# Kernel optimization log

Measured on AMD Instinct MI355X. Metric: run time of the kernel, lower is better.

The kernel has to match this reference:

```python
import jax, jax.numpy as jnp
import numpy as np

TOKENS = 8192
IN_FEATURES = 4096
OUT_FEATURES = 4096
ALPHA = 2e-05
BETA = 8.0


def setup_inputs() -> dict:
    key = jax.random.key(0)
    kx, kw = jax.random.split(key)
    # int8 activations and weights, values in [-127, 127]
    x = jax.random.randint(kx, (TOKENS, IN_FEATURES), -127, 128, dtype=jnp.int32).astype(jnp.int8)
    weight = jax.random.randint(kw, (OUT_FEATURES, IN_FEATURES), -127, 128, dtype=jnp.int32).astype(jnp.int8)
    bias = jnp.zeros((OUT_FEATURES,), dtype=jnp.float32)
    a = jnp.float32(ALPHA)  # dequant scale: input_scale * weight_scale
    b = jnp.float32(BETA)   # requant scale: 1 / out_scale
    return {"x": x, "weight": weight, "bias": bias, "a": a, "b": b}


def reference(x, weight, bias, a, b):
    acc = jnp.matmul(x.astype(jnp.int32), weight.T.astype(jnp.int32))
    # fp32 epilogue: dequant scale + bias, exact GeLU, requant by beta
    y = a * acc.astype(jnp.float32) + bias[None, :]
    y = jax.nn.gelu(y, approximate=False)
    # quantize output to int8 (round to nearest even, saturate)
    q = jnp.clip(jnp.rint(y * b), -128.0, 127.0).astype(jnp.int8)
    return q
```

## Files before the change

kernel.cpp:

```cpp
#include <hip/hip_runtime.h>
#include <cstdint>
#include <cstddef>

#define TOKENS 8192
#define INF    4096
#define OUTF   4096

typedef int v4i __attribute__((ext_vector_type(4)));

__global__ __launch_bounds__(256) void pack_i8_kernel(
    const int* __restrict__ xi, const int* __restrict__ wi,
    uint8_t* __restrict__ x8, uint8_t* __restrict__ w8) {
  const int NXT = (TOKENS * INF) / 16;
  const int NT  = 2048 * 256;
  int tid = blockIdx.x * 256 + threadIdx.x;
#pragma unroll 1
  for (int g = 0; g < 6; ++g) {
    int t = g * NT + tid;
    const int4* s;
    int4* d;
    if (t < NXT) {
      s = (const int4*)xi + 4 * (size_t)t;
      d = (int4*)x8 + t;
    } else {
      int t2 = t - NXT;
      s = (const int4*)wi + 4 * (size_t)t2;
      d = (int4*)w8 + t2;
    }
    int4 v0 = s[0], v1 = s[1], v2 = s[2], v3 = s[3];
    int4 p;
    p.x = (v0.x & 255) | ((v0.y & 255) << 8) | ((v0.z & 255) << 16) | (v0.w << 24);
    p.y = (v1.x & 255) | ((v1.y & 255) << 8) | ((v1.z & 255) << 16) | (v1.w << 24);
    p.z = (v2.x & 255) | ((v2.y & 255) << 8) | ((v2.z & 255) << 16) | (v2.w << 24);
    p.w = (v3.x & 255) | ((v3.y & 255) << 8) | ((v3.z & 255) << 16) | (v3.w << 24);
    *d = p;
  }
}

__device__ __forceinline__ float gelu_exact(float y) {
  float x = y * 0.70710678118654752f;
  float s = fabsf(x);
  float t = __builtin_amdgcn_rcpf(fmaf(s, 0.3275911f, 1.0f));
  float p = t * fmaf(t, fmaf(t, fmaf(t, fmaf(t, 1.061405429f, -1.453152027f),
                                     1.421413741f), -0.284496736f),
                     0.254829592f);
  float e = __expf(-s * s);
  float er = fmaf(-p, e, 1.0f);
  er = copysignf(er, x);
  return 0.5f * y * (1.0f + er);
}

__device__ __forceinline__ void barrier_fenced() {
  asm volatile("" ::: "memory");
  __builtin_amdgcn_s_barrier();
  asm volatile("" ::: "memory");
}

__global__ __launch_bounds__(512, 2) void gemm_i8_gelu_q_kernel(
    const uint8_t* __restrict__ x8, const uint8_t* __restrict__ w8,
    const float* __restrict__ bias, const float* __restrict__ pa,
    const float* __restrict__ pb, int* __restrict__ out) {
  __shared__ char sm[131072];

  const int tid = threadIdx.x;
  const int l   = tid & 63;
  const int wv  = tid >> 6;
  const int wr  = wv >> 2;
  const int wc  = wv & 3;
  const int lr  = l & 15;
  const int lg  = l >> 4;

  int id = blockIdx.x;
  int wg = (id & 7) * 64 + (id >> 3);
  const int m0 = (wg >> 4) * 256;
  const int n0 = (wg & 15) * 256;

  const float av = pa[0];
  const float bv = pb[0];

  const int grow = (wv << 5) + (l >> 3);
  const int gch  = ((l & 7) ^ ((l >> 3) & 7)) << 4;
  const uint8_t* gA = x8 + (size_t)(m0 + grow) * INF + gch;
  const uint8_t* gB = w8 + (size_t)(n0 + grow) * INF + gch;
  const int dwv = wv * 4096;

  int aoff[8], boff[4], sb0, sb1;
#pragma unroll
  for (int m = 0; m < 8; ++m) aoff[m] = (wr * 128 + m * 16 + lr) * 128;
#pragma unroll
  for (int n = 0; n < 4; ++n) boff[n] = 32768 + (wc * 64 + n * 16 + lr) * 128;
  sb0 = ((0 + lg) ^ (l & 7)) << 4;
  sb1 = ((4 + lg) ^ (l & 7)) << 4;

  v4i acc[8][4];
#pragma unroll
  for (int m = 0; m < 8; ++m)
#pragma unroll
    for (int n = 0; n < 4; ++n) acc[m][n] = (v4i){0, 0, 0, 0};

#define GLL(gsrc, ldst)                                                       \
  __builtin_amdgcn_global_load_lds(                                           \
      (const __attribute__((address_space(1))) unsigned*)(gsrc),              \
      (__attribute__((address_space(3))) unsigned*)(ldst), 16, 0, 0);

#define GLA(T, J) GLL(gA + (size_t)(J) * 8 * INF + (size_t)(T) * 128,         \
                      sm + (((T) & 1) << 16) + dwv + (J) * 1024)
#define GLB(T, J) GLL(gB + (size_t)(J) * 8 * INF + (size_t)(T) * 128,         \
                      sm + (((T) & 1) << 16) + 32768 + dwv + (J) * 1024)

#define LD(off) (*(const v4i*)(sbr + (off)))
#define MM(ACC, AF, BF)                                                       \
  ACC = __builtin_amdgcn_mfma_i32_16x16x64_i8(AF, BF, ACC, 0, 0, 0)

#define KSTEP                                                                 \
  __builtin_amdgcn_s_setprio(1);                                              \
  MM(acc[0][0], A0[0], B0[0]); MM(acc[0][1], A0[0], B0[1]);                   \
  MM(acc[1][0], A0[1], B0[0]); MM(acc[1][1], A0[1], B0[1]);                   \
  MM(acc[2][0], A0[2], B0[0]); MM(acc[2][1], A0[2], B0[1]);                   \
  MM(acc[3][0], A0[3], B0[0]); MM(acc[3][1], A0[3], B0[1]);                   \
  __builtin_amdgcn_s_setprio(0);                                              \
  __builtin_amdgcn_s_setprio(1);                                              \
  MM(acc[4][0], A4[0], B0[0]); MM(acc[4][1], A4[0], B0[1]);                   \
  MM(acc[5][0], A4[1], B0[0]); MM(acc[5][1], A4[1], B0[1]);                   \
  MM(acc[6][0], A4[2], B0[0]); MM(acc[6][1], A4[2], B0[1]);                   \
  MM(acc[7][0], A4[3], B0[0]); MM(acc[7][1], A4[3], B0[1]);                   \
  __builtin_amdgcn_s_setprio(0);                                              \
  __builtin_amdgcn_s_setprio(1);                                              \
  MM(acc[0][2], A0[0], B2[0]); MM(acc[0][3], A0[0], B2[1]);                   \
  MM(acc[1][2], A0[1], B2[0]); MM(acc[1][3], A0[1], B2[1]);                   \
  MM(acc[2][2], A0[2], B2[0]); MM(acc[2][3], A0[2], B2[1]);                   \
  MM(acc[3][2], A0[3], B2[0]); MM(acc[3][3], A0[3], B2[1]);                   \
  __builtin_amdgcn_s_setprio(0);                                              \
  __builtin_amdgcn_s_setprio(1);                                              \
  MM(acc[4][2], A4[0], B2[0]); MM(acc[4][3], A4[0], B2[1]);                   \
  MM(acc[5][2], A4[1], B2[0]); MM(acc[5][3], A4[1], B2[1]);                   \
  MM(acc[6][2], A4[2], B2[0]); MM(acc[6][3], A4[2], B2[1]);                   \
  MM(acc[7][2], A4[3], B2[0]); MM(acc[7][3], A4[3], B2[1]);                   \
  __builtin_amdgcn_s_setprio(0);

#define ITER(DS)                                                              \
  {                                                                           \
    const char* sbr = sm + ((kt & 1) << 16);                                  \
    const int T = kt + 1;                                                     \
    v4i A0[4], A4[4], B0[2], B2[2];                                           \
        \
    A0[0] = LD(aoff[0] + sb0); A0[1] = LD(aoff[1] + sb0);                     \
    A0[2] = LD(aoff[2] + sb0); A0[3] = LD(aoff[3] + sb0);                     \
    B0[0] = LD(boff[0] + sb0); B0[1] = LD(boff[1] + sb0);                     \
    if (DS) {                                                                 \
      GLA(T, 0); GLA(T, 1); GLA(T, 2); GLA(T, 3);                             \
      GLB(T, 0); GLB(T, 1); GLB(T, 2); GLB(T, 3);                             \
    }                                                                         \
    A4[0] = LD(aoff[4] + sb0); A4[1] = LD(aoff[5] + sb0);                     \
    A4[2] = LD(aoff[6] + sb0); A4[3] = LD(aoff[7] + sb0);                     \
    B2[0] = LD(boff[2] + sb0); B2[1] = LD(boff[3] + sb0);                     \
    KSTEP                                                                     \
    A0[0] = LD(aoff[0] + sb1); A0[1] = LD(aoff[1] + sb1);                     \
    A0[2] = LD(aoff[2] + sb1); A0[3] = LD(aoff[3] + sb1);                     \
    B0[0] = LD(boff[0] + sb1); B0[1] = LD(boff[1] + sb1);                     \
    A4[0] = LD(aoff[4] + sb1); A4[1] = LD(aoff[5] + sb1);                     \
    A4[2] = LD(aoff[6] + sb1); A4[3] = LD(aoff[7] + sb1);                     \
    B2[0] = LD(boff[2] + sb1); B2[1] = LD(boff[3] + sb1);                     \
    KSTEP                                                                     \
          \
    if (DS) { asm volatile("s_waitcnt vmcnt(0)" ::: "memory"); }              \
    barrier_fenced();                                                         \
  }

  GLA(0, 0); GLA(0, 1); GLA(0, 2); GLA(0, 3);
  GLB(0, 0); GLB(0, 1); GLB(0, 2); GLB(0, 3);
  asm volatile("s_waitcnt vmcnt(0)" ::: "memory");
  barrier_fenced();

#pragma unroll 1
  for (int kt = 0; kt < 31; ++kt) ITER(1)
  {
    const int kt = 31;
    ITER(0)
  }

  float bvals[4];
#pragma unroll
  for (int n = 0; n < 4; ++n) bvals[n] = bias[n0 + wc * 64 + n * 16 + lr];

#pragma unroll
  for (int m = 0; m < 8; ++m) {
    int rowb = m0 + wr * 128 + m * 16 + lg * 4;
#pragma unroll
    for (int q = 0; q < 4; ++q) {
      size_t rb = (size_t)(rowb + q) * OUTF;
#pragma unroll
      for (int n = 0; n < 4; ++n) {
        float f = fmaf(av, (float)acc[m][n][q], bvals[n]);
        float g = gelu_exact(f);
        float r = __builtin_rintf(g * bv);
        r = fminf(fmaxf(r, -128.0f), 127.0f);
        out[rb + (size_t)(n0 + wc * 64 + n * 16 + lr)] = (int)r;
      }
    }
  }
#undef GLL
#undef GLA
#undef GLB
#undef LD
#undef MM
#undef KSTEP
#undef ITER
}

extern "C" void kernel_launch(void* const* d_in, const int* in_sizes, int n_in,
                              void* d_out, int out_size, void* d_ws,
                              size_t ws_size, hipStream_t stream) {
  const int*   xi   = (const int*)d_in[0];
  const int*   wi   = (const int*)d_in[1];
  const float* bias = (const float*)d_in[2];
  const float* pa   = (const float*)d_in[3];
  const float* pb   = (const float*)d_in[4];
  int*         out  = (int*)d_out;

  uint8_t* x8 = (uint8_t*)d_ws;
  uint8_t* w8 = x8 + (size_t)TOKENS * INF;

  pack_i8_kernel<<<2048, 256, 0, stream>>>(xi, wi, x8, w8);

  dim3 grid((TOKENS / 256) * (OUTF / 256));
  gemm_i8_gelu_q_kernel<<<grid, 512, 0, stream>>>(x8, w8, bias, pa, pb, out);
}
```

Measured before the change: 388.0 us.

## Interleave LDS fragment loads with MFMA clusters and pin schedule with group barriers

Moves the wait-and-barrier to the start of each k-tile iteration, so the global-to-LDS prefetch for the next tile is issued right after the barrier. The second half-step's A/B fragment loads are split and interleaved between MFMA clusters using separate register sets. sched_group_barrier directives pin the order of global loads, LDS reads and MFMAs. The aim is to hide LDS read latency behind matrix work, at the cost of more live vector registers, which could reduce occupancy or cause spills.

```diff
diff --git a/kernel.cpp b/kernel.cpp
--- a/kernel.cpp
+++ b/kernel.cpp
@@ -112,65 +112,58 @@
 #define MM(ACC, AF, BF)                                                       \
   ACC = __builtin_amdgcn_mfma_i32_16x16x64_i8(AF, BF, ACC, 0, 0, 0)
 
-#define KSTEP                                                                 \
+#define CL(AF, BF, MB, NB)                                                    \
   __builtin_amdgcn_s_setprio(1);                                              \
-  MM(acc[0][0], A0[0], B0[0]); MM(acc[0][1], A0[0], B0[1]);                   \
-  MM(acc[1][0], A0[1], B0[0]); MM(acc[1][1], A0[1], B0[1]);                   \
-  MM(acc[2][0], A0[2], B0[0]); MM(acc[2][1], A0[2], B0[1]);                   \
-  MM(acc[3][0], A0[3], B0[0]); MM(acc[3][1], A0[3], B0[1]);                   \
-  __builtin_amdgcn_s_setprio(0);                                              \
-  __builtin_amdgcn_s_setprio(1);                                              \
-  MM(acc[4][0], A4[0], B0[0]); MM(acc[4][1], A4[0], B0[1]);                   \
-  MM(acc[5][0], A4[1], B0[0]); MM(acc[5][1], A4[1], B0[1]);                   \
-  MM(acc[6][0], A4[2], B0[0]); MM(acc[6][1], A4[2], B0[1]);                   \
-  MM(acc[7][0], A4[3], B0[0]); MM(acc[7][1], A4[3], B0[1]);                   \
-  __builtin_amdgcn_s_setprio(0);                                              \
-  __builtin_amdgcn_s_setprio(1);                                              \
-  MM(acc[0][2], A0[0], B2[0]); MM(acc[0][3], A0[0], B2[1]);                   \
-  MM(acc[1][2], A0[1], B2[0]); MM(acc[1][3], A0[1], B2[1]);                   \
-  MM(acc[2][2], A0[2], B2[0]); MM(acc[2][3], A0[2], B2[1]);                   \
-  MM(acc[3][2], A0[3], B2[0]); MM(acc[3][3], A0[3], B2[1]);                   \
-  __builtin_amdgcn_s_setprio(0);                                              \
-  __builtin_amdgcn_s_setprio(1);                                              \
-  MM(acc[4][2], A4[0], B2[0]); MM(acc[4][3], A4[0], B2[1]);                   \
-  MM(acc[5][2], A4[1], B2[0]); MM(acc[5][3], A4[1], B2[1]);                   \
-  MM(acc[6][2], A4[2], B2[0]); MM(acc[6][3], A4[2], B2[1]);                   \
-  MM(acc[7][2], A4[3], B2[0]); MM(acc[7][3], A4[3], B2[1]);                   \
+  MM(acc[(MB)+0][(NB)+0], AF[0], BF[0]); MM(acc[(MB)+0][(NB)+1], AF[0], BF[1]);\
+  MM(acc[(MB)+1][(NB)+0], AF[1], BF[0]); MM(acc[(MB)+1][(NB)+1], AF[1], BF[1]);\
+  MM(acc[(MB)+2][(NB)+0], AF[2], BF[0]); MM(acc[(MB)+2][(NB)+1], AF[2], BF[1]);\
+  MM(acc[(MB)+3][(NB)+0], AF[3], BF[0]); MM(acc[(MB)+3][(NB)+1], AF[3], BF[1]);\
   __builtin_amdgcn_s_setprio(0);
 
 #define ITER(DS)                                                              \
   {                                                                           \
     const char* sbr = sm + ((kt & 1) << 16);                                  \
     const int T = kt + 1;                                                     \
-    v4i A0[4], A4[4], B0[2], B2[2];                                           \
-        \
-    A0[0] = LD(aoff[0] + sb0); A0[1] = LD(aoff[1] + sb0);                     \
-    A0[2] = LD(aoff[2] + sb0); A0[3] = LD(aoff[3] + sb0);                     \
-    B0[0] = LD(boff[0] + sb0); B0[1] = LD(boff[1] + sb0);                     \
+    asm volatile("s_waitcnt vmcnt(0)" ::: "memory");      \
+    barrier_fenced();           \
     if (DS) {                                                                 \
       GLA(T, 0); GLA(T, 1); GLA(T, 2); GLA(T, 3);                             \
       GLB(T, 0); GLB(T, 1); GLB(T, 2); GLB(T, 3);                             \
     }                                                                         \
-    A4[0] = LD(aoff[4] + sb0); A4[1] = LD(aoff[5] + sb0);                     \
-    A4[2] = LD(aoff[6] + sb0); A4[3] = LD(aoff[7] + sb0);                     \
-    B2[0] = LD(boff[2] + sb0); B2[1] = LD(boff[3] + sb0);                     \
-    KSTEP                                                                     \
-    A0[0] = LD(aoff[0] + sb1); A0[1] = LD(aoff[1] + sb1);                     \
-    A0[2] = LD(aoff[2] + sb1); A0[3] = LD(aoff[3] + sb1);                     \
-    B0[0] = LD(boff[0] + sb1); B0[1] = LD(boff[1] + sb1);                     \
-    A4[0] = LD(aoff[4] + sb1); A4[1] = LD(aoff[5] + sb1);                     \
-    A4[2] = LD(aoff[6] + sb1); A4[3] = LD(aoff[7] + sb1);                     \
-    B2[0] = LD(boff[2] + sb1); B2[1] = LD(boff[3] + sb1);                     \
-    KSTEP                                                                     \
-          \
-    if (DS) { asm volatile("s_waitcnt vmcnt(0)" ::: "memory"); }              \
-    barrier_fenced();                                                         \
+    v4i a0[4], a4[4], b0[2], b2[2];                             \
+    v4i c0[4], c4[4], d0[2], d2[2];             \
+    a0[0] = LD(aoff[0] + sb0); a0[1] = LD(aoff[1] + sb0);                     \
+    a0[2] = LD(aoff[2] + sb0); a0[3] = LD(aoff[3] + sb0);                     \
+    b0[0] = LD(boff[0] + sb0); b0[1] = LD(boff[1] + sb0);                     \
+    a4[0] = LD(aoff[4] + sb0); a4[1] = LD(aoff[5] + sb0);                     \
+    a4[2] = LD(aoff[6] + sb0); a4[3] = LD(aoff[7] + sb0);                     \
+    b2[0] = LD(boff[2] + sb0); b2[1] = LD(boff[3] + sb0);                     \
+    CL(a0, b0, 0, 0)                                                          \
+    c0[0] = LD(aoff[0] + sb1); c0[1] = LD(aoff[1] + sb1);                     \
+    c0[2] = LD(aoff[2] + sb1); c0[3] = LD(aoff[3] + sb1);                     \
+    d0[0] = LD(boff[0] + sb1); d0[1] = LD(boff[1] + sb1);                     \
+    CL(a4, b0, 4, 0)                                                          \
+    CL(a0, b2, 0, 2)                                                          \
+    c4[0] = LD(aoff[4] + sb1); c4[1] = LD(aoff[5] + sb1);                     \
+    c4[2] = LD(aoff[6] + sb1); c4[3] = LD(aoff[7] + sb1);                     \
+    d2[0] = LD(boff[2] + sb1); d2[1] = LD(boff[3] + sb1);                     \
+    CL(a4, b2, 4, 2)                                                          \
+    CL(c0, d0, 0, 0)                                                          \
+    CL(c4, d0, 4, 0)                                                          \
+    CL(c0, d2, 0, 2)                                                          \
+    CL(c4, d2, 4, 2)                                                          \
+     \
+    if (DS) { __builtin_amdgcn_sched_group_barrier(0x020, 8, 0); }            \
+    __builtin_amdgcn_sched_group_barrier(0x100, 12, 0);                       \
+    __builtin_amdgcn_sched_group_barrier(0x008, 8, 0);                        \
+    __builtin_amdgcn_sched_group_barrier(0x100, 6, 0);                        \
+    __builtin_amdgcn_sched_group_barrier(0x008, 16, 0);                       \
+    __builtin_amdgcn_sched_group_barrier(0x100, 6, 0);                        \
+    __builtin_amdgcn_sched_group_barrier(0x008, 40, 0);                       \
   }
 
   GLA(0, 0); GLA(0, 1); GLA(0, 2); GLA(0, 3);
   GLB(0, 0); GLB(0, 1); GLB(0, 2); GLB(0, 3);
-  asm volatile("s_waitcnt vmcnt(0)" ::: "memory");
-  barrier_fenced();
 
 #pragma unroll 1
   for (int kt = 0; kt < 31; ++kt) ITER(1)
@@ -204,7 +197,7 @@
 #undef GLB
 #undef LD
 #undef MM
-#undef KSTEP
+#undef CL
 #undef ITER
 }
 
```

Result: no change. 385.6 us (-0.6%).
